# Kernel tuning notes

Hardware: AMD Instinct MI355X
Metric: run time of the kernel (lower is better)

The kernel has to match this reference:

```python
import jax, jax.numpy as jnp
import numpy as np

HIDDEN = 2048
HEADS = 16
HEAD_DIM = HIDDEN // HEADS


def setup_inputs() -> dict:
    key = jax.random.key(0)
    ks = jax.random.split(key, 9)
    s = 1.0 / np.sqrt(HIDDEN)
    return {
        "hidden_states": jax.random.normal(ks[0], (2, 2048, HIDDEN), dtype=jnp.float32),
        "wq": jax.random.uniform(ks[1], (HIDDEN, HIDDEN), jnp.float32, -s, s),
        "bq": jax.random.uniform(ks[2], (HIDDEN,), jnp.float32, -s, s),
        "wk": jax.random.uniform(ks[3], (HIDDEN, HIDDEN), jnp.float32, -s, s),
        "bk": jax.random.uniform(ks[4], (HIDDEN,), jnp.float32, -s, s),
        "wv": jax.random.uniform(ks[5], (HIDDEN, HIDDEN), jnp.float32, -s, s),
        "bv": jax.random.uniform(ks[6], (HIDDEN,), jnp.float32, -s, s),
        "wo": jax.random.uniform(ks[7], (HIDDEN, HIDDEN), jnp.float32, -s, s),
        "bo": jax.random.uniform(ks[8], (HIDDEN,), jnp.float32, -s, s),
    }


def reference(hidden_states, wq, bq, wk, bk, wv, bv, wo, bo):
    B, S, _ = hidden_states.shape
    # QKV projections (nn.Linear: x @ W^T + b)
    q = hidden_states @ wq.T + bq
    k = hidden_states @ wk.T + bk
    v = hidden_states @ wv.T + bv
    # [B, S, H, D] -> [B, H, S, D]
    q = q.reshape(B, S, HEADS, HEAD_DIM).transpose(0, 2, 1, 3)
    k = k.reshape(B, S, HEADS, HEAD_DIM).transpose(0, 2, 1, 3)
    v = v.reshape(B, S, HEADS, HEAD_DIM).transpose(0, 2, 1, 3)
    scale = HEAD_DIM ** (-0.5)
    scores = jnp.einsum("bhqd,bhkd->bhqk", q, k) * scale  # [B,H,S,S]
    attn = jax.nn.softmax(scores, axis=-1)
    out = jnp.einsum("bhqk,bhkd->bhqd", attn, v)
    out = out.transpose(0, 2, 1, 3).reshape(B, S, HIDDEN)
    return out @ wo.T + bo
```

## Files before the change

kernel.cpp:

```cpp
#include <hip/hip_runtime.h>
#include <math.h>

#define HID 2048
#define NB  2
#define SEQ 2048
#define NT  (NB*SEQ)
#define NH  16
#define HD  128

typedef __attribute__((ext_vector_type(8))) _Float16 f16x8;
typedef __attribute__((ext_vector_type(2))) __fp16   h16x2;
typedef __attribute__((ext_vector_type(4))) float    f32x4;

#define QSCALE 0.12751742f

__device__ __forceinline__ unsigned short f2h(float x) {
    union { _Float16 h; unsigned short u; } c;
    c.h = (_Float16)x;
    return c.u;
}

extern "C" __global__ __launch_bounds__(256)
void cast_x(const float* __restrict__ src, unsigned short* __restrict__ dst, int n4)
{
    const int i = blockIdx.x * 256 + threadIdx.x;
    if (i >= n4) return;
    const float4 x = ((const float4*)src)[i];
    ushort4 h;
    h.x = f2h(x.x); h.y = f2h(x.y); h.z = f2h(x.z); h.w = f2h(x.w);
    ((ushort4*)dst)[i] = h;
}

extern "C" __global__ __launch_bounds__(256)
void cast_w4(const float* __restrict__ s0, const float* __restrict__ s1,
             const float* __restrict__ s2, const float* __restrict__ s3,
             unsigned short* __restrict__ d0, unsigned short* __restrict__ d1,
             unsigned short* __restrict__ d2, unsigned short* __restrict__ d3,
             int n4)
{
    const int which = blockIdx.y;
    const float* __restrict__ src =
        (which==0) ? s0 : (which==1) ? s1 : (which==2) ? s2 : s3;
    unsigned short* __restrict__ dst =
        (which==0) ? d0 : (which==1) ? d1 : (which==2) ? d2 : d3;
    const int i = blockIdx.x * 256 + threadIdx.x;
    if (i >= n4) return;
    const float4 x = ((const float4*)src)[i];
    ushort4 h;
    h.x = f2h(x.x); h.y = f2h(x.y); h.z = f2h(x.z); h.w = f2h(x.w);
    ((ushort4*)dst)[i] = h;
}

extern "C" __global__ __launch_bounds__(256)
void qkv_f16(const unsigned short* __restrict__ Xh,
             const unsigned short* __restrict__ Wqh,
             const unsigned short* __restrict__ Wkh,
             const unsigned short* __restrict__ Wvh,
             const float* __restrict__ bq, const float* __restrict__ bk,
             const float* __restrict__ bv,
             unsigned short* __restrict__ Qb, unsigned short* __restrict__ Kb,
             unsigned short* __restrict__ Vb)
{
    const int on0 = blockIdx.x * 128;
    const int tm0 = blockIdx.y * 128;
    const int which = blockIdx.z;
    const unsigned short* __restrict__ W = (which==0) ? Wqh : (which==1) ? Wkh : Wvh;
    const float* __restrict__ bias      = (which==0) ? bq  : (which==1) ? bk  : bv;

    __shared__ unsigned short Ah[8192], Bh[8192];

    const int tid  = threadIdx.x;
    const int lane = tid & 63;
    const int w    = tid >> 6;
    const int wm   = (w & 1) * 64;
    const int wn   = (w >> 1) * 64;
    const int fr   = lane & 15;
    const int quad = lane >> 4;

    f32x4 acc[4][4];
    #pragma unroll
    for (int i = 0; i < 4; ++i)
        #pragma unroll
        for (int j = 0; j < 4; ++j)
            acc[i][j] = (f32x4){0.f, 0.f, 0.f, 0.f};

    for (int kb = 0; kb < HID/64; ++kb) {
        __syncthreads();
        const unsigned short* Asrc = Xh + (size_t)tm0*HID + kb*64;
        const unsigned short* Bsrc = W  + (size_t)on0*HID + kb*64;
        #pragma unroll
        for (int r = 0; r < 4; ++r) {
            const int p   = (r*4 + w)*64 + lane;
            const int row = p >> 3;
            const int c   = (p & 7) ^ (row & 7);
            __builtin_amdgcn_global_load_lds(
                (const __attribute__((address_space(1))) void*)(Asrc + (size_t)row*HID + c*8),
                (__attribute__((address_space(3))) void*)(Ah + (r*4 + w)*512), 16, 0, 0);
            __builtin_amdgcn_global_load_lds(
                (const __attribute__((address_space(1))) void*)(Bsrc + (size_t)row*HID + c*8),
                (__attribute__((address_space(3))) void*)(Bh + (r*4 + w)*512), 16, 0, 0);
        }
        __syncthreads();

        #pragma unroll
        for (int kk = 0; kk < 2; ++kk) {
            f16x8 a[4], b[4];
            #pragma unroll
            for (int i = 0; i < 4; ++i) {
                const int ra = wm + i*16 + fr;
                a[i] = *(const f16x8*)(Ah + (ra*8 + ((kk*4 + quad) ^ (ra & 7)))*8);
                const int rb = wn + i*16 + fr;
                b[i] = *(const f16x8*)(Bh + (rb*8 + ((kk*4 + quad) ^ (rb & 7)))*8);
            }
            #pragma unroll
            for (int i = 0; i < 4; ++i)
                #pragma unroll
                for (int j = 0; j < 4; ++j)
                    acc[i][j] = __builtin_amdgcn_mfma_f32_16x16x32_f16(a[i], b[j], acc[i][j], 0, 0, 0);
        }
    }

    const int col_l = fr;
    if (which == 2) {
        #pragma unroll
        for (int j = 0; j < 4; ++j) {
            const int o = on0 + wn + j*16 + col_l;
            const float bb = bias[o];
            const int h = o >> 7, d = o & (HD-1);
            #pragma unroll
            for (int i = 0; i < 4; ++i)
                #pragma unroll
                for (int rg = 0; rg < 4; ++rg) {
                    const int t = tm0 + wm + i*16 + quad*4 + rg;
                    const int b = t >> 11, s = t & (SEQ-1);
                    const int pos = (s & ~63) | (((s & 15) << 2) | ((s >> 4) & 3));
                    Vb[((size_t)(b*NH + h)*HD + d)*SEQ + pos] = f2h(acc[i][j][rg] + bb);
                }
        }
    } else {
        const float sc = (which == 0) ? QSCALE : 1.0f;
        unsigned short* __restrict__ dstp = (which == 0) ? Qb : Kb;
        #pragma unroll
        for (int j = 0; j < 4; ++j) {
            const int o = on0 + wn + j*16 + col_l;
            const float bb = bias[o];
            const int h = o >> 7, d = o & (HD-1);
            #pragma unroll
            for (int i = 0; i < 4; ++i)
                #pragma unroll
                for (int rg = 0; rg < 4; ++rg) {
                    const int t = tm0 + wm + i*16 + quad*4 + rg;
                    const int b = t >> 11, s = t & (SEQ-1);
                    dstp[((size_t)(b*NH + h)*SEQ + s)*HD + d] =
                        f2h((acc[i][j][rg] + bb) * sc);
                }
        }
    }
}

#define PS_STRIDE 72

extern "C" __global__ __launch_bounds__(512, 4)
void attn_mfma(const unsigned short* __restrict__ Qg, const unsigned short* __restrict__ Kg,
               const unsigned short* __restrict__ Vtg, unsigned short* __restrict__ Of)
{
    const int L  = blockIdx.x;
    const int q0 = (L >> 5) * 128;
    const int bh = ((L & 7) << 2) | ((L >> 3) & 3);
    const unsigned short* __restrict__ Qp = Qg  + (size_t)bh * SEQ * HD;
    const unsigned short* __restrict__ Kp = Kg  + (size_t)bh * SEQ * HD;
    const unsigned short* __restrict__ Vp = Vtg + (size_t)bh * HD * SEQ;

    __shared__ alignas(16) unsigned short Ks[64*128];
    __shared__ alignas(16) unsigned short Vts[128*64];
    __shared__ alignas(16) unsigned short Ps[8][16*PS_STRIDE];

    const int tid  = threadIdx.x;
    const int lane = tid & 63;
    const int w    = tid >> 6;
    const int fr   = lane & 15;
    const int quad = lane >> 4;

    f16x8 qf[4];
    #pragma unroll
    for (int c = 0; c < 4; ++c)
        qf[c] = *(const f16x8*)(Qp + (size_t)(q0 + w*16 + fr)*HD + c*32 + quad*8);

    f32x4 accO[8];
    #pragma unroll
    for (int n = 0; n < 8; ++n)
        accO[n] = (f32x4){0.f, 0.f, 0.f, 0.f};
    float lp[4] = {};

    for (int kt = 0; kt < SEQ/64; ++kt) {
        __syncthreads();
        {
            const unsigned short* Kt = Kp + (size_t)kt*64*HD;
            #pragma unroll
            for (int r = 0; r < 2; ++r) {
                const int p   = (r*8 + w)*64 + lane;
                const int row = p >> 4;
                const int c   = (p & 15) ^ (row & 15);
                __builtin_amdgcn_global_load_lds(
                    (const __attribute__((address_space(1))) void*)(Kt + (size_t)row*HD + c*8),
                    (__attribute__((address_space(3))) void*)(Ks + (r*8 + w)*512), 16, 0, 0);
            }
            #pragma unroll
            for (int r = 0; r < 2; ++r) {
                const int p   = (r*8 + w)*64 + lane;
                const int row = p >> 3;
                const int c   = (p & 7) ^ (row & 7);
                __builtin_amdgcn_global_load_lds(
                    (const __attribute__((address_space(1))) void*)(Vp + (size_t)row*SEQ + kt*64 + c*8),
                    (__attribute__((address_space(3))) void*)(Vts + (r*8 + w)*512), 16, 0, 0);
            }
        }
        __syncthreads();

        f32x4 accS[4];
        #pragma unroll
        for (int n = 0; n < 4; ++n)
            accS[n] = (f32x4){0.f, 0.f, 0.f, 0.f};
        #pragma unroll
        for (int c = 0; c < 4; ++c) {
            f16x8 bf[4];
            #pragma unroll
            for (int n = 0; n < 4; ++n)
                bf[n] = *(const f16x8*)(Ks + (n*16 + fr)*128 + ((c*4 + quad) ^ fr)*8);
            __builtin_amdgcn_s_setprio(1);
            #pragma unroll
            for (int n = 0; n < 4; ++n)
                accS[n] = __builtin_amdgcn_mfma_f32_16x16x32_f16(
                    qf[c], bf[n], accS[n], 0, 0, 0);
            __builtin_amdgcn_s_setprio(0);
        }

        #pragma unroll
        for (int rg = 0; rg < 4; ++rg) {
            float p0 = exp2f(accS[0][rg]);
            float p1 = exp2f(accS[1][rg]);
            float p2 = exp2f(accS[2][rg]);
            float p3 = exp2f(accS[3][rg]);
            lp[rg] += (p0 + p1) + (p2 + p3);
            union { h16x2 h[2]; ushort4 u4; } pk;
            pk.h[0] = __builtin_amdgcn_cvt_pkrtz(p0, p1);
            pk.h[1] = __builtin_amdgcn_cvt_pkrtz(p2, p3);
            *(ushort4*)(&Ps[w][(quad*4 + rg)*PS_STRIDE + fr*4]) = pk.u4;
        }

        #pragma unroll
        for (int cc = 0; cc < 2; ++cc) {
            f16x8 pf = *(const f16x8*)(&Ps[w][fr*PS_STRIDE + cc*32 + quad*8]);
            f16x8 vf[8];
            #pragma unroll
            for (int n = 0; n < 8; ++n)
                vf[n] = *(const f16x8*)(Vts + (n*16 + fr)*64 + ((cc*4 + quad) ^ (fr & 7))*8);
            __builtin_amdgcn_s_setprio(1);
            #pragma unroll
            for (int n = 0; n < 8; ++n)
                accO[n] = __builtin_amdgcn_mfma_f32_16x16x32_f16(
                    pf, vf[n], accO[n], 0, 0, 0);
            __builtin_amdgcn_s_setprio(0);
        }
    }

    float inv[4];
    #pragma unroll
    for (int rg = 0; rg < 4; ++rg) {
        float l = lp[rg];
        l += __shfl_xor(l, 1);
        l += __shfl_xor(l, 2);
        l += __shfl_xor(l, 4);
        l += __shfl_xor(l, 8);
        inv[rg] = 1.0f / l;
    }
    const int bb_ = bh >> 4;
    const int hh_ = bh & (NH - 1);
    #pragma unroll
    for (int n = 0; n < 8; ++n) {
        const int d = n*16 + fr;
        #pragma unroll
        for (int rg = 0; rg < 4; ++rg) {
            const int s = q0 + w*16 + quad*4 + rg;
            Of[((size_t)(bb_*SEQ + s))*HID + hh_*HD + d] = f2h(accO[n][rg] * inv[rg]);
        }
    }
}

extern "C" __global__ __launch_bounds__(512)
void oproj_f16(const unsigned short* __restrict__ Af,
               const unsigned short* __restrict__ Woh,
               const float* __restrict__ bo, float* __restrict__ Y)
{
    const int on0 = blockIdx.x * 128;
    const int tm0 = blockIdx.y * 128;

    __shared__ unsigned short Ah[8192], Bh[8192];

    const int tid  = threadIdx.x;
    const int lane = tid & 63;
    const int w    = tid >> 6;
    const int wm   = (w >> 2) * 64;
    const int wn   = (w & 3) * 32;
    const int fr   = lane & 15;
    const int quad = lane >> 4;

    f32x4 acc[4][2];
    #pragma unroll
    for (int i = 0; i < 4; ++i)
        #pragma unroll
        for (int j = 0; j < 2; ++j)
            acc[i][j] = (f32x4){0.f, 0.f, 0.f, 0.f};

    for (int kb = 0; kb < HID/64; ++kb) {
        __syncthreads();
        const unsigned short* Asrc = Af  + (size_t)tm0*HID + kb*64;
        const unsigned short* Bsrc = Woh + (size_t)on0*HID + kb*64;
        #pragma unroll
        for (int r = 0; r < 2; ++r) {
            const int p   = r*512 + tid;
            const int row = p >> 3;
            const int c   = (p & 7) ^ (row & 7);
            __builtin_amdgcn_global_load_lds(
                (const __attribute__((address_space(1))) void*)(Asrc + (size_t)row*HID + c*8),
                (__attribute__((address_space(3))) void*)(Ah + p*8), 16, 0, 0);
            __builtin_amdgcn_global_load_lds(
                (const __attribute__((address_space(1))) void*)(Bsrc + (size_t)row*HID + c*8),
                (__attribute__((address_space(3))) void*)(Bh + p*8), 16, 0, 0);
        }
        __syncthreads();

        #pragma unroll
        for (int kk = 0; kk < 2; ++kk) {
            f16x8 a[4], b[2];
            #pragma unroll
            for (int i = 0; i < 4; ++i) {
                const int ra = wm + i*16 + fr;
                a[i] = *(const f16x8*)(Ah + (ra*8 + ((kk*4 + quad) ^ (ra & 7)))*8);
            }
            #pragma unroll
            for (int j = 0; j < 2; ++j) {
                const int rb = wn + j*16 + fr;
                b[j] = *(const f16x8*)(Bh + (rb*8 + ((kk*4 + quad) ^ (rb & 7)))*8);
            }
            #pragma unroll
            for (int i = 0; i < 4; ++i)
                #pragma unroll
                for (int j = 0; j < 2; ++j)
                    acc[i][j] = __builtin_amdgcn_mfma_f32_16x16x32_f16(a[i], b[j], acc[i][j], 0, 0, 0);
        }
    }

    #pragma unroll
    for (int j = 0; j < 2; ++j) {
        const int o = on0 + wn + j*16 + fr;
        const float bb = bo[o];
        #pragma unroll
        for (int i = 0; i < 4; ++i)
            #pragma unroll
            for (int rg = 0; rg < 4; ++rg) {
                const int t = tm0 + wm + i*16 + quad*4 + rg;
                Y[(size_t)t*HID + o] = acc[i][j][rg] + bb;
            }
    }
}

extern "C" void kernel_launch(void* const* d_in, const int* in_sizes, int n_in,
                              void* d_out, int out_size, void* d_ws, size_t ws_size,
                              hipStream_t stream)
{
    const float* X  = (const float*)d_in[0];
    const float* wq = (const float*)d_in[1];
    const float* bq = (const float*)d_in[2];
    const float* wk = (const float*)d_in[3];
    const float* bk = (const float*)d_in[4];
    const float* wv = (const float*)d_in[5];
    const float* bv = (const float*)d_in[6];
    const float* wo = (const float*)d_in[7];
    const float* bo = (const float*)d_in[8];
    float* Y = (float*)d_out;

    const size_t F  = (size_t)NT * HID;
    const size_t Wn = (size_t)HID * HID;

    unsigned short* Qb  = (unsigned short*)d_ws;
    unsigned short* Kb  = Qb  + F;
    unsigned short* Vb  = Kb  + F;
    unsigned short* Of  = Vb  + F;
    unsigned short* Xh  = Of  + F;
    unsigned short* Wqh = Xh  + F;
    unsigned short* Wkh = Wqh + Wn;
    unsigned short* Wvh = Wkh + Wn;
    unsigned short* Woh = Wvh + Wn;

    cast_x<<<(int)(F/4/256), 256, 0, stream>>>(X, Xh, (int)(F/4));
    cast_w4<<<dim3((int)(Wn/4/256), 4), 256, 0, stream>>>(
        wq, wk, wv, wo, Wqh, Wkh, Wvh, Woh, (int)(Wn/4));

    qkv_f16<<<dim3(HID/128, NT/128, 3), 256, 0, stream>>>(
        Xh, Wqh, Wkh, Wvh, bq, bk, bv, Qb, Kb, Vb);

    attn_mfma<<<dim3(512, 1, 1), 512, 0, stream>>>(Qb, Kb, Vb, Of);

    oproj_f16<<<dim3(HID/128, NT/128), 512, 0, stream>>>(Of, Woh, bo, Y);
}
```

Baseline: 402.8 us.

## Register-prefetch next K/V tile in attention and merge cast kernels

```diff
diff --git a/kernel.cpp b/kernel.cpp
--- a/kernel.cpp
+++ b/kernel.cpp
@@ -8,9 +8,10 @@
 #define NH  16
 #define HD  128
 
-typedef __attribute__((ext_vector_type(8))) _Float16 f16x8;
-typedef __attribute__((ext_vector_type(2))) __fp16   h16x2;
-typedef __attribute__((ext_vector_type(4))) float    f32x4;
+typedef __attribute__((ext_vector_type(8))) _Float16       f16x8;
+typedef __attribute__((ext_vector_type(8))) unsigned short u16x8;
+typedef __attribute__((ext_vector_type(2))) __fp16         h16x2;
+typedef __attribute__((ext_vector_type(4))) float          f32x4;
 
 #define QSCALE 0.12751742f
 
@@ -21,28 +22,20 @@
 }
 
 extern "C" __global__ __launch_bounds__(256)
-void cast_x(const float* __restrict__ src, unsigned short* __restrict__ dst, int n4)
+void cast_all(const float* __restrict__ X,
+              const float* __restrict__ w0, const float* __restrict__ w1,
+              const float* __restrict__ w2, const float* __restrict__ w3,
+              unsigned short* __restrict__ Xd,
+              unsigned short* __restrict__ d0, unsigned short* __restrict__ d1,
+              unsigned short* __restrict__ d2, unsigned short* __restrict__ d3,
+              int n4x, int n4w)
 {
-    const int i = blockIdx.x * 256 + threadIdx.x;
-    if (i >= n4) return;
-    const float4 x = ((const float4*)src)[i];
-    ushort4 h;
-    h.x = f2h(x.x); h.y = f2h(x.y); h.z = f2h(x.z); h.w = f2h(x.w);
-    ((ushort4*)dst)[i] = h;
-}
-
-extern "C" __global__ __launch_bounds__(256)
-void cast_w4(const float* __restrict__ s0, const float* __restrict__ s1,
-             const float* __restrict__ s2, const float* __restrict__ s3,
-             unsigned short* __restrict__ d0, unsigned short* __restrict__ d1,
-             unsigned short* __restrict__ d2, unsigned short* __restrict__ d3,
-             int n4)
-{
-    const int which = blockIdx.y;
+    const int y = blockIdx.y;
     const float* __restrict__ src =
-        (which==0) ? s0 : (which==1) ? s1 : (which==2) ? s2 : s3;
+        (y==0) ? X : (y==1) ? w0 : (y==2) ? w1 : (y==3) ? w2 : w3;
     unsigned short* __restrict__ dst =
-        (which==0) ? d0 : (which==1) ? d1 : (which==2) ? d2 : d3;
+        (y==0) ? Xd : (y==1) ? d0 : (y==2) ? d1 : (y==3) ? d2 : d3;
+    const int n4 = (y==0) ? n4x : n4w;
     const int i = blockIdx.x * 256 + threadIdx.x;
     if (i >= n4) return;
     const float4 x = ((const float4*)src)[i];
@@ -192,30 +185,42 @@
         accO[n] = (f32x4){0.f, 0.f, 0.f, 0.f};
     float lp[4] = {};
 
+    u16x8 kreg[2], vreg[2];
+
+    int kp_[2], krow_[2], kc_[2];
+    int vp_[2], vrow_[2], vc_[2];
+    #pragma unroll
+    for (int r = 0; r < 2; ++r) {
+        const int p = (r*8 + w)*64 + lane;
+        kp_[r] = p; krow_[r] = p >> 4; kc_[r] = (p & 15) ^ (krow_[r] & 15);
+        vp_[r] = p; vrow_[r] = p >> 3; vc_[r] = (p & 7) ^ (vrow_[r] & 7);
+    }
+
+#define ISSUE_KV(kt_) do {                                                     \
+    const unsigned short* _Kt = Kp + (size_t)(kt_)*64*HD;                      \
+    _Pragma("unroll")                                                          \
+    for (int _r = 0; _r < 2; ++_r)                                             \
+        kreg[_r] = *(const u16x8*)(_Kt + (size_t)krow_[_r]*HD + kc_[_r]*8);    \
+    _Pragma("unroll")                                                          \
+    for (int _r = 0; _r < 2; ++_r)                                             \
+        vreg[_r] = *(const u16x8*)(Vp + (size_t)vrow_[_r]*SEQ + (kt_)*64 + vc_[_r]*8); \
+    } while (0)
+
+#define WRITE_KV() do {                                                        \
+    _Pragma("unroll")                                                          \
+    for (int _r = 0; _r < 2; ++_r)                                             \
+        *(u16x8*)(Ks + kp_[_r]*8) = kreg[_r];                                  \
+    _Pragma("unroll")                                                          \
+    for (int _r = 0; _r < 2; ++_r)                                             \
+        *(u16x8*)(Vts + vp_[_r]*8) = vreg[_r];                                 \
+    } while (0)
+
+    ISSUE_KV(0);
+    WRITE_KV();
+    __syncthreads();
+
     for (int kt = 0; kt < SEQ/64; ++kt) {
-        __syncthreads();
-        {
-            const unsigned short* Kt = Kp + (size_t)kt*64*HD;
-            #pragma unroll
-            for (int r = 0; r < 2; ++r) {
-                const int p   = (r*8 + w)*64 + lane;
-                const int row = p >> 4;
-                const int c   = (p & 15) ^ (row & 15);
-                __builtin_amdgcn_global_load_lds(
-                    (const __attribute__((address_space(1))) void*)(Kt + (size_t)row*HD + c*8),
-                    (__attribute__((address_space(3))) void*)(Ks + (r*8 + w)*512), 16, 0, 0);
-            }
-            #pragma unroll
-            for (int r = 0; r < 2; ++r) {
-                const int p   = (r*8 + w)*64 + lane;
-                const int row = p >> 3;
-                const int c   = (p & 7) ^ (row & 7);
-                __builtin_amdgcn_global_load_lds(
-                    (const __attribute__((address_space(1))) void*)(Vp + (size_t)row*SEQ + kt*64 + c*8),
-                    (__attribute__((address_space(3))) void*)(Vts + (r*8 + w)*512), 16, 0, 0);
-            }
-        }
-        __syncthreads();
+        if (kt + 1 < SEQ/64) ISSUE_KV(kt + 1);
 
         f32x4 accS[4];
         #pragma unroll
@@ -262,7 +267,13 @@
                     pf, vf[n], accO[n], 0, 0, 0);
             __builtin_amdgcn_s_setprio(0);
         }
-    }
+
+        __syncthreads();
+        if (kt + 1 < SEQ/64) WRITE_KV();
+        __syncthreads();
+    }
+#undef ISSUE_KV
+#undef WRITE_KV
 
     float inv[4];
     #pragma unroll
@@ -393,9 +404,11 @@
     unsigned short* Wvh = Wkh + Wn;
     unsigned short* Woh = Wvh + Wn;
 
-    cast_x<<<(int)(F/4/256), 256, 0, stream>>>(X, Xh, (int)(F/4));
-    cast_w4<<<dim3((int)(Wn/4/256), 4), 256, 0, stream>>>(
-        wq, wk, wv, wo, Wqh, Wkh, Wvh, Woh, (int)(Wn/4));
+    const int n4x = (int)(F/4);
+    const int n4w = (int)(Wn/4);
+
+    cast_all<<<dim3((n4x + 255)/256, 5), 256, 0, stream>>>(
+        X, wq, wk, wv, wo, Xh, Wqh, Wkh, Wvh, Woh, n4x, n4w);
 
     qkv_f16<<<dim3(HID/128, NT/128, 3), 256, 0, stream>>>(
         Xh, Wqh, Wkh, Wvh, bq, bk, bv, Qb, Kb, Vb);
```

After: 412.6 us. 1.02x slower.
